# Optimization experiments

Hardware: AMD Instinct MI355X
Metric: run time of the kernel (lower is better)

The kernel has to match this reference:

```python
import jax, jax.numpy as jnp
import numpy as np

BN_EPS = 1e-5


def setup_inputs() -> dict:
    key = jax.random.key(0)
    k1, k2 = jax.random.split(key)
    B, IN, OUT = 16384, 2048, 2048
    x = jax.random.normal(k1, (B, IN), dtype=jnp.float32)
    weight = jax.random.normal(k2, (OUT, IN), dtype=jnp.float32) * 0.05
    gamma = jnp.ones((OUT,), dtype=jnp.float32)
    beta = jnp.zeros((OUT,), dtype=jnp.float32)
    return {"x": x, "weight": weight, "gamma": gamma, "beta": beta}


def reference(x, weight, gamma, beta):
    # Deterministic binarization: sign(w) in {-1, +1} (0 maps to +1)
    w_bin = jnp.where(weight >= 0, 1.0, -1.0).astype(weight.dtype)
    # Linear (no bias): y = x @ W_bin^T  -> [B, OUT]
    y = jnp.einsum("bi,oi->bo", x, w_bin)
    # BatchNorm1d, training mode: biased batch statistics over batch dim
    mean = jnp.mean(y, axis=0)
    var = jnp.mean(jnp.square(y - mean), axis=0)
    y = (y - mean) * (gamma * jax.lax.rsqrt(var + BN_EPS)) + beta
    # ReLU activation
    return jax.nn.relu(y)
```

## Files before the change

### kernel.cpp

```cpp
#include <hip/hip_runtime.h>
#include <stdint.h>

#define B_DIM   16384
#define IN_DIM  2048
#define OUT_DIM 2048
#define BN_EPS  1e-5f

typedef int    i32x4 __attribute__((ext_vector_type(4)));
typedef unsigned short u16x4 __attribute__((ext_vector_type(4)));


__device__ __forceinline__ unsigned short f2bf_rne(float f) {
    unsigned u = __builtin_bit_cast(unsigned, f);
    return (unsigned short)((u + 0x7fffu + ((u >> 16) & 1u)) >> 16);
}
__device__ __forceinline__ float bf2f(unsigned short h) {
    unsigned u = ((unsigned)h) << 16;
    return __builtin_bit_cast(float, u);
}

__device__ __forceinline__ void gl_lds16(const void* g, void* l) {
    __builtin_amdgcn_global_load_lds(
        (const __attribute__((address_space(1))) unsigned int*)g,
        (__attribute__((address_space(3))) unsigned int*)l,
        16, 0, 0);
}

__device__ __forceinline__ int pack4(float a, float b, float c, float d, float inv) {
    int q0 = (int)rintf(a * inv) & 255;
    int q1 = (int)rintf(b * inv) & 255;
    int q2 = (int)rintf(c * inv) & 255;
    int q3 = (int)rintf(d * inv) & 255;
    return q0 | (q1 << 8) | (q2 << 16) | (q3 << 24);
}

__global__ __launch_bounds__(256) void quantize_x_kernel(
        const float4* __restrict__ x4, int* __restrict__ xq,
        float* __restrict__ scales) {
    __shared__ float wmax[4];
    const int row = blockIdx.x;
    const int t = threadIdx.x;
    const float4* xr = x4 + (size_t)row * 512;
    float4 a = xr[t];
    float4 b = xr[t + 256];
    float m = fmaxf(fmaxf(fabsf(a.x), fabsf(a.y)), fmaxf(fabsf(a.z), fabsf(a.w)));
    m = fmaxf(m, fmaxf(fmaxf(fabsf(b.x), fabsf(b.y)), fmaxf(fabsf(b.z), fabsf(b.w))));
#pragma unroll
    for (int off = 32; off >= 1; off >>= 1) m = fmaxf(m, __shfl_xor(m, off));
    if ((t & 63) == 0) wmax[t >> 6] = m;
    __syncthreads();
    m = fmaxf(fmaxf(wmax[0], wmax[1]), fmaxf(wmax[2], wmax[3]));
    m = fmaxf(m, 1e-20f);
    const float inv = 127.0f / m;
    if (t == 0) scales[row] = m * (1.0f / 127.0f);
    int* xo = xq + (size_t)row * 512;
    xo[t]       = pack4(a.x, a.y, a.z, a.w, inv);
    xo[t + 256] = pack4(b.x, b.y, b.z, b.w, inv);
}

__global__ __launch_bounds__(256) void convert_w_kernel(
        const float4* __restrict__ w, int* __restrict__ wq,
        float4* __restrict__ stats ) {
    int id = blockIdx.x * 256 + threadIdx.x;
    if (id < 1024) stats[id] = make_float4(0.f, 0.f, 0.f, 0.f);
    float4 a = w[id];
    int b0 = (a.x < 0.f) ? 0xFF : 0x01;
    int b1 = (a.y < 0.f) ? 0xFF : 0x01;
    int b2 = (a.z < 0.f) ? 0xFF : 0x01;
    int b3 = (a.w < 0.f) ? 0xFF : 0x01;
    wq[id] = b0 | (b1 << 8) | (b2 << 16) | (b3 << 24);
}

__global__ __launch_bounds__(256, 2) void gemm_bn_kernel(
        const char* __restrict__ A, const char* __restrict__ Bw,
        const float* __restrict__ scales,
        unsigned short* __restrict__ Yb,
        float* __restrict__ colsum, float* __restrict__ colsumsq) {
    __shared__ char sA[2 * 128 * 64];
    __shared__ char sB[2 * 128 * 64];

    const int tid  = threadIdx.x;
    const int wave = tid >> 6;
    const int lane = tid & 63;
    const int wm = wave >> 1;
    const int wn = wave & 1;
    const int lr = lane & 15;
    const int lq = lane >> 4;

    const int b  = blockIdx.x;
    const int lb = (b & 7) * 256 + (b >> 3);
    const int bm = (lb >> 4) * 128;
    const int bn = (lb & 15) * 128;

    const int srow = lane >> 2;
    const int scol = (lane & 3) * 16;
    const char* gp[8];
    char* lp[8];
#pragma unroll
    for (int q = 0; q < 8; ++q) {
        int g    = wave * 8 + q;
        int isB  = g >> 4;
        int slab = (g >> 3) & 1;
        int c    = g & 7;
        const char* basep = isB ? Bw : A;
        int tileoff       = isB ? bn : bm;
        gp[q] = basep + (size_t)(tileoff + c * 16 + srow) * IN_DIM
                      + slab * 64 + scol;
        char* sbase = isB ? sB : sA;
        lp[q] = sbase + slab * 8192 + c * 1024 + lane * 16;
    }

    const int aoff = (wm * 64 + lr) * 64 + lq * 16;
    const int boff = (wn * 64 + lr) * 64 + lq * 16;

    i32x4 acc[4][4];
#pragma unroll
    for (int i = 0; i < 4; ++i)
#pragma unroll
        for (int j = 0; j < 4; ++j) {
            i32x4 z = {0, 0, 0, 0};
            acc[i][j] = z;
        }

    for (int k0 = 0; k0 < IN_DIM; k0 += 128) {
        __syncthreads();
#pragma unroll
        for (int q = 0; q < 8; ++q)
            gl_lds16(gp[q] + k0, lp[q]);
        __syncthreads();

#pragma unroll
        for (int kh = 0; kh < 2; ++kh) {
            const char* aB = sA + kh * 8192 + aoff;
            const char* bB = sB + kh * 8192 + boff;
            i32x4 av[4], bv[4];
#pragma unroll
            for (int i = 0; i < 4; ++i)
                av[i] = *(const i32x4*)(aB + i * 1024);
#pragma unroll
            for (int j = 0; j < 4; ++j)
                bv[j] = *(const i32x4*)(bB + j * 1024);
#pragma unroll
            for (int i = 0; i < 4; ++i)
#pragma unroll
                for (int j = 0; j < 4; ++j)
                    acc[i][j] = __builtin_amdgcn_mfma_i32_16x16x64_i8(
                        av[i], bv[j], acc[i][j], 0, 0, 0);
        }
    }

    float colS[4], colQ[4];
#pragma unroll
    for (int j = 0; j < 4; ++j) { colS[j] = 0.f; colQ[j] = 0.f; }

#pragma unroll
    for (int i = 0; i < 4; ++i) {
        const int row0 = bm + wm * 64 + i * 16 + lq * 4;
        float sc[4];
#pragma unroll
        for (int r = 0; r < 4; ++r) sc[r] = scales[row0 + r];
#pragma unroll
        for (int r = 0; r < 4; ++r) {
            size_t base = (size_t)(row0 + r) * OUT_DIM + bn + wn * 64 + lr;
#pragma unroll
            for (int j = 0; j < 4; ++j) {
                float v = (float)acc[i][j][r] * sc[r];
                Yb[base + j * 16] = f2bf_rne(v);
                colS[j] += v;
                colQ[j] += v * v;
            }
        }
    }

#pragma unroll
    for (int j = 0; j < 4; ++j) {
        float s = colS[j], q = colQ[j];
        s += __shfl_xor(s, 16); s += __shfl_xor(s, 32);
        q += __shfl_xor(q, 16); q += __shfl_xor(q, 32);
        if (lq == 0) {
            int col = bn + wn * 64 + j * 16 + lr;
            atomicAdd(&colsum[col], s);
            atomicAdd(&colsumsq[col], q);
        }
    }
}

__global__ __launch_bounds__(256) void finalize_kernel(
        const float* __restrict__ colsum, const float* __restrict__ colsumsq,
        const float* __restrict__ gamma, const float* __restrict__ beta,
        float* __restrict__ scale, float* __restrict__ bias) {
    int n = blockIdx.x * 256 + threadIdx.x;
    if (n < OUT_DIM) {
        const float inv = 1.f / (float)B_DIM;
        float mean = colsum[n] * inv;
        float var  = colsumsq[n] * inv - mean * mean;
        float sc   = gamma[n] * rsqrtf(var + BN_EPS);
        scale[n] = sc;
        bias[n]  = beta[n] - mean * sc;
    }
}

__global__ __launch_bounds__(256) void bn_relu_bf16_kernel(
        const u16x4* __restrict__ yb, float4* __restrict__ out,
        const float4* __restrict__ scale4, const float4* __restrict__ bias4) {
    int base = blockIdx.x * 512 + threadIdx.x;
#pragma unroll
    for (int p = 0; p < 2; ++p) {
        int id = base + p * 256;
        int c4 = id & (OUT_DIM / 4 - 1);
        u16x4 h = yb[id];
        float4 s = scale4[c4];
        float4 bb = bias4[c4];
        float4 v;
        v.x = fmaxf(fmaf(bf2f(h[0]), s.x, bb.x), 0.f);
        v.y = fmaxf(fmaf(bf2f(h[1]), s.y, bb.y), 0.f);
        v.z = fmaxf(fmaf(bf2f(h[2]), s.z, bb.z), 0.f);
        v.w = fmaxf(fmaf(bf2f(h[3]), s.w, bb.w), 0.f);
        out[id] = v;
    }
}

extern "C" void kernel_launch(void* const* d_in, const int* in_sizes, int n_in,
                              void* d_out, int out_size, void* d_ws, size_t ws_size,
                              hipStream_t stream) {
    const float* x     = (const float*)d_in[0];
    const float* w     = (const float*)d_in[1];
    const float* gamma = (const float*)d_in[2];
    const float* beta  = (const float*)d_in[3];
    float* out = (float*)d_out;

    char* ws = (char*)d_ws;
    const size_t XQ_OFF = 0;
    const size_t WQ_OFF = XQ_OFF + (size_t)B_DIM * IN_DIM;
    const size_t YB_OFF = WQ_OFF + (size_t)OUT_DIM * IN_DIM;
    const size_t ST_OFF = YB_OFF + (size_t)B_DIM * OUT_DIM * 2;
    const size_t SC_OFF = ST_OFF + 8192 * 4;

    char* xq = ws + XQ_OFF;
    char* wq = ws + WQ_OFF;
    unsigned short* yb = (unsigned short*)(ws + YB_OFF);
    float* colsum   = (float*)(ws + ST_OFF);
    float* colsumsq = colsum + 2048;
    float* scale    = colsum + 4096;
    float* bias     = colsum + 6144;
    float* scales   = (float*)(ws + SC_OFF);

    quantize_x_kernel<<<B_DIM, 256, 0, stream>>>(
        (const float4*)x, (int*)xq, scales);
    convert_w_kernel<<<4096, 256, 0, stream>>>(
        (const float4*)w, (int*)wq, (float4*)colsum);
    gemm_bn_kernel<<<2048, 256, 0, stream>>>(
        xq, wq, scales, yb, colsum, colsumsq);
    finalize_kernel<<<8, 256, 0, stream>>>(
        colsum, colsumsq, gamma, beta, scale, bias);
    bn_relu_bf16_kernel<<<16384, 256, 0, stream>>>(
        (const u16x4*)yb, (float4*)out, (const float4*)scale,
        (const float4*)bias);
}
```

Before: 328.2 us.

## Switch int8 GEMM to 32x32x32 MFMA with XOR-swizzled LDS layout

Replaces the 4x4 grid of 16x16x64 int8 MFMAs per wave with a 2x2 grid of 32x32x32 MFMAs, halving LDS fragment loads per k-step and using the larger-tile instruction. Adds an XOR swizzle on the 16-byte column chunks, both in the global-to-LDS copy and in the fragment reads, to avoid LDS bank conflicts under the new 32-row access pattern. The epilogue and column-statistics reduction are remapped to the 32x32 accumulator layout. The remapping is error-prone, and the epilogue's stores and scale loads now follow a different per-lane pattern.

```diff
diff --git a/kernel.cpp b/kernel.cpp
--- a/kernel.cpp
+++ b/kernel.cpp
@@ -6,7 +6,8 @@
 #define OUT_DIM 2048
 #define BN_EPS  1e-5f
 
-typedef int    i32x4 __attribute__((ext_vector_type(4)));
+typedef int    i32x4  __attribute__((ext_vector_type(4)));
+typedef int    i32x16 __attribute__((ext_vector_type(16)));
 typedef unsigned short u16x4 __attribute__((ext_vector_type(4)));
 
 
@@ -84,8 +85,9 @@
     const int lane = tid & 63;
     const int wm = wave >> 1;
     const int wn = wave & 1;
-    const int lr = lane & 15;
-    const int lq = lane >> 4;
+    const int r  = lane & 31;
+    const int hw = lane >> 5;
+    const int swz = (r ^ (r >> 2)) & 3;
 
     const int b  = blockIdx.x;
     const int lb = (b & 7) * 256 + (b >> 3);
@@ -93,7 +95,8 @@
     const int bn = (lb & 15) * 128;
 
     const int srow = lane >> 2;
-    const int scol = (lane & 3) * 16;
+    const int fsw  = ((srow ^ (srow >> 2)) & 3) << 4;
+    const int scol = (((lane & 3) << 4)) ^ fsw;
     const char* gp[8];
     char* lp[8];
 #pragma unroll
@@ -110,17 +113,16 @@
         lp[q] = sbase + slab * 8192 + c * 1024 + lane * 16;
     }
 
-    const int aoff = (wm * 64 + lr) * 64 + lq * 16;
-    const int boff = (wn * 64 + lr) * 64 + lq * 16;
-
-    i32x4 acc[4][4];
-#pragma unroll
-    for (int i = 0; i < 4; ++i)
-#pragma unroll
-        for (int j = 0; j < 4; ++j) {
-            i32x4 z = {0, 0, 0, 0};
-            acc[i][j] = z;
-        }
+    const int arow = (wm * 64 + r) * 64;
+    const int brow = (wn * 64 + r) * 64;
+
+    i32x16 acc[2][2];
+#pragma unroll
+    for (int i = 0; i < 2; ++i)
+#pragma unroll
+        for (int j = 0; j < 2; ++j)
+#pragma unroll
+            for (int e = 0; e < 16; ++e) acc[i][j][e] = 0;
 
     for (int k0 = 0; k0 < IN_DIM; k0 += 128) {
         __syncthreads();
@@ -130,55 +132,45 @@
         __syncthreads();
 
 #pragma unroll
-        for (int kh = 0; kh < 2; ++kh) {
-            const char* aB = sA + kh * 8192 + aoff;
-            const char* bB = sB + kh * 8192 + boff;
-            i32x4 av[4], bv[4];
-#pragma unroll
-            for (int i = 0; i < 4; ++i)
-                av[i] = *(const i32x4*)(aB + i * 1024);
-#pragma unroll
-            for (int j = 0; j < 4; ++j)
-                bv[j] = *(const i32x4*)(bB + j * 1024);
-#pragma unroll
-            for (int i = 0; i < 4; ++i)
-#pragma unroll
-                for (int j = 0; j < 4; ++j)
-                    acc[i][j] = __builtin_amdgcn_mfma_i32_16x16x64_i8(
-                        av[i], bv[j], acc[i][j], 0, 0, 0);
+        for (int ks = 0; ks < 4; ++ks) {
+            const int slab = (ks >> 1) * 8192;
+            const int col  = ((((ks & 1) << 1) | hw) ^ swz) << 4;
+            i32x4 a0 = *(const i32x4*)(sA + slab + arow + col);
+            i32x4 a1 = *(const i32x4*)(sA + slab + arow + 2048 + col);
+            i32x4 b0 = *(const i32x4*)(sB + slab + brow + col);
+            i32x4 b1 = *(const i32x4*)(sB + slab + brow + 2048 + col);
+            acc[0][0] = __builtin_amdgcn_mfma_i32_32x32x32_i8(a0, b0, acc[0][0], 0, 0, 0);
+            acc[0][1] = __builtin_amdgcn_mfma_i32_32x32x32_i8(a0, b1, acc[0][1], 0, 0, 0);
+            acc[1][0] = __builtin_amdgcn_mfma_i32_32x32x32_i8(a1, b0, acc[1][0], 0, 0, 0);
+            acc[1][1] = __builtin_amdgcn_mfma_i32_32x32x32_i8(a1, b1, acc[1][1], 0, 0, 0);
         }
     }
 
-    float colS[4], colQ[4];
-#pragma unroll
-    for (int j = 0; j < 4; ++j) { colS[j] = 0.f; colQ[j] = 0.f; }
-
-#pragma unroll
-    for (int i = 0; i < 4; ++i) {
-        const int row0 = bm + wm * 64 + i * 16 + lq * 4;
-        float sc[4];
-#pragma unroll
-        for (int r = 0; r < 4; ++r) sc[r] = scales[row0 + r];
-#pragma unroll
-        for (int r = 0; r < 4; ++r) {
-            size_t base = (size_t)(row0 + r) * OUT_DIM + bn + wn * 64 + lr;
-#pragma unroll
-            for (int j = 0; j < 4; ++j) {
-                float v = (float)acc[i][j][r] * sc[r];
-                Yb[base + j * 16] = f2bf_rne(v);
+    float colS[2] = {0.f, 0.f}, colQ[2] = {0.f, 0.f};
+#pragma unroll
+    for (int i = 0; i < 2; ++i) {
+        const int row0 = bm + wm * 64 + i * 32 + hw * 4;
+#pragma unroll
+        for (int reg = 0; reg < 16; ++reg) {
+            const int row = row0 + (reg & 3) + ((reg >> 2) << 3);
+            const float sc = scales[row];
+            size_t base = (size_t)row * OUT_DIM + bn + wn * 64 + r;
+#pragma unroll
+            for (int j = 0; j < 2; ++j) {
+                float v = (float)acc[i][j][reg] * sc;
+                Yb[base + j * 32] = f2bf_rne(v);
                 colS[j] += v;
                 colQ[j] += v * v;
             }
         }
     }
-
-#pragma unroll
-    for (int j = 0; j < 4; ++j) {
+#pragma unroll
+    for (int j = 0; j < 2; ++j) {
         float s = colS[j], q = colQ[j];
-        s += __shfl_xor(s, 16); s += __shfl_xor(s, 32);
-        q += __shfl_xor(q, 16); q += __shfl_xor(q, 32);
-        if (lq == 0) {
-            int col = bn + wn * 64 + j * 16 + lr;
+        s += __shfl_xor(s, 32);
+        q += __shfl_xor(q, 32);
+        if (hw == 0) {
+            int col = bn + wn * 64 + j * 32 + r;
             atomicAdd(&colsum[col], s);
             atomicAdd(&colsumsq[col], q);
         }
```

Measured after the change: 333.4 us. About the same (+1.6%).
